# Performance work log

Hardware: AMD Instinct MI355X
Metric: run time of the kernel (lower is better)

## Reference

```python
import jax, jax.numpy as jnp
import numpy as np

BASE = 257
HASH_MOD = 4096
WINDOWS = (2, 4, 8, 16)
MATCH_OFFSETS = (1, 2, 4, 8)
CHUNK = 32
EPS_LN = 1e-5


def _shift_right(x, k):
    # (B,T) -> shifted right by k along time, zero-filled
    B, T = x.shape
    return jnp.concatenate([jnp.zeros((B, k), x.dtype), x[:, :T - k]], axis=1)


def _rolling_hashes(chars):
    # polynomial rolling hash over each window size, mod HASH_MOD -> (B,T,S) int32
    c = chars.astype(jnp.int32)
    hs = []
    for w in WINDOWS:
        acc = jnp.zeros_like(c)
        p = 1
        for j in range(w):  # small fixed loop (<=16)
            acc = acc + _shift_right(c, j) * p
            p = (p * BASE) % HASH_MOD
        hs.append(acc % HASH_MOD)
    return jnp.stack(hs, axis=2)


def _match_features(chars):
    feats = []
    for k in MATCH_OFFSETS:
        m = (chars == _shift_right(chars, k)).astype(jnp.float32)
        m = m.at[:, :k].set(0.0)
        feats.append(m)
    return jnp.stack(feats, axis=-1)  # (B,T,n_match)


def _layer_norm(x, g, b):
    mu = jnp.mean(x, axis=-1, keepdims=True)
    var = jnp.mean((x - mu) ** 2, axis=-1, keepdims=True)
    return (x - mu) * jax.lax.rsqrt(var + EPS_LN) * g + b


def _forward(chars, emb_byte, hash_tables, Wq, bq, conv_w, conv_b, Win, b_in,
             Wg, bg, Wi, bi, Wo, bo, ln_g, ln_b, mlp_w, mlp_b, Wout, bout):
    B, T = chars.shape
    byte_emb = emb_byte[chars]                       # (B,T,Eb)
    hidx = _rolling_hashes(chars)                    # (B,T,S)
    scale_embeds = jnp.stack(
        [hash_tables[s][hidx[:, :, s]] for s in range(len(WINDOWS))], axis=2
    )                                                # (B,T,S,E)
    # scale attention: query from byte embedding, softmax over scales
    E = scale_embeds.shape[-1]
    q = byte_emb @ Wq + bq                           # (B,T,E)
    scores = jnp.einsum('bte,btse->bts', q, scale_embeds) / jnp.sqrt(jnp.float32(E))
    w = jax.nn.softmax(scores, axis=-1)
    hash_feat = jnp.einsum('bts,btse->bte', w, scale_embeds)
    # causal depthwise conv + silu
    C = hash_feat.shape[-1]
    kk = conv_w.shape[-1]
    ht = jnp.moveaxis(hash_feat, 1, 2)               # (B,C,T)
    ht = jnp.pad(ht, ((0, 0), (0, 0), (kk - 1, 0)))
    ht = jax.lax.conv_general_dilated(
        ht, conv_w, window_strides=(1,), padding='VALID',
        dimension_numbers=('NCH', 'OIH', 'NCH'), feature_group_count=C)
    hash_feat = jax.nn.silu(jnp.moveaxis(ht + conv_b[None, :, None], 2, 1))
    mf = _match_features(chars)
    feat = jnp.concatenate([byte_emb, hash_feat, mf], axis=-1)
    h = jax.nn.silu(feat @ Win + b_in)               # (B,T,H)
    # TinyScan: chunked log-space gated scan, carry across chunks via lax.scan
    gates = jax.nn.sigmoid(h @ Wg + bg)              # (B,T,S)
    drive = (1.0 - gates) * (h @ Wi + bi)
    S = gates.shape[-1]
    nC = T // CHUNK
    g = gates.reshape(B, nC, CHUNK, S).transpose(1, 0, 2, 3)
    d = drive.reshape(B, nC, CHUNK, S).transpose(1, 0, 2, 3)

    def step(hc, ab):
        a, b = ab                                    # (B,K,S)
        log_a = jnp.log(jnp.maximum(a, 1e-6))
        cum_a = jnp.exp(jnp.cumsum(log_a, axis=1))
        inv = 1.0 / jnp.maximum(cum_a, 1e-8)
        cum_wb = jnp.cumsum(b * inv, axis=1)
        out = cum_a * (hc[:, None, :] + cum_wb)
        return out[:, -1], out

    _, states = jax.lax.scan(step, jnp.zeros((B, S), h.dtype), (g, d))
    states = states.transpose(1, 0, 2, 3).reshape(B, T, S)
    h = _layer_norm(h + states @ Wo + bo, ln_g, ln_b)
    # residual MLP blocks: x + silu(Linear(x))
    for l in range(mlp_w.shape[0]):
        h = h + jax.nn.silu(h @ mlp_w[l] + mlp_b[l])
    return h @ Wout + bout                           # (B,T,V)


def setup_inputs() -> dict:
    key = jax.random.key(0)
    ks = jax.random.split(key, 12)
    B, T, V = 8, 8192, 256
    EB, E, H, SS, KC, NM, NR = 64, 64, 512, 32, 4, 4, 3
    feat = EB + E + NM

    def lin(k, i, o):
        return (jax.random.normal(k, (i, o), jnp.float32) / np.sqrt(i)).astype(jnp.float32)

    return {
        'chars': jax.random.randint(ks[0], (B, T), 0, V),
        'emb_byte': jax.random.normal(ks[1], (V, EB), jnp.float32) * 0.02,
        'hash_tables': jax.random.normal(ks[2], (len(WINDOWS), HASH_MOD, E), jnp.float32) * 0.02,
        'Wq': lin(ks[3], EB, E), 'bq': jnp.zeros((E,), jnp.float32),
        'conv_w': jax.random.normal(ks[4], (E, 1, KC), jnp.float32) * 0.2,
        'conv_b': jnp.zeros((E,), jnp.float32),
        'Win': lin(ks[5], feat, H), 'b_in': jnp.zeros((H,), jnp.float32),
        'Wg': lin(ks[6], H, SS), 'bg': jnp.zeros((SS,), jnp.float32),
        'Wi': lin(ks[7], H, SS), 'bi': jnp.zeros((SS,), jnp.float32),
        'Wo': lin(ks[8], SS, H), 'bo': jnp.zeros((H,), jnp.float32),
        'ln_g': jnp.ones((H,), jnp.float32), 'ln_b': jnp.zeros((H,), jnp.float32),
        'mlp_w': jax.random.normal(ks[9], (NR, H, H), jnp.float32) / np.sqrt(H),
        'mlp_b': jnp.zeros((NR, H), jnp.float32),
        'Wout': lin(ks[10], H, V), 'bout': jnp.zeros((V,), jnp.float32),
    }


def reference(chars, emb_byte, hash_tables, Wq, bq, conv_w, conv_b, Win, b_in,
              Wg, bg, Wi, bi, Wo, bo, ln_g, ln_b, mlp_w, mlp_b, Wout, bout):
    return _forward(chars, emb_byte, hash_tables, Wq, bq, conv_w, conv_b, Win, b_in,
                    Wg, bg, Wi, bi, Wo, bo, ln_g, ln_b, mlp_w, mlp_b, Wout, bout)
```

## Files before the change

### kernel.cpp

```cpp
#include <hip/hip_runtime.h>
#include <hip/hip_bf16.h>
#include <math.h>

#define B_ 8
#define T_ 8192
#define V_ 256
#define EB_ 64
#define E_ 64
#define H_ 512
#define SS_ 32
#define FEATP_ 192
#define NCH_ 256
#define CHUNK_ 32

typedef __attribute__((ext_vector_type(8))) short bf8;
typedef __attribute__((ext_vector_type(16))) float accv;

#define AS1(p) (__attribute__((address_space(1))) void*)(void*)(p)
#define AS3(p) (__attribute__((address_space(3))) void*)(void*)(p)

__device__ __forceinline__ float silu_f(float x) { return x / (1.0f + expf(-x)); }
__device__ __forceinline__ float sigm_f(float x) { return 1.0f / (1.0f + expf(-x)); }
__device__ __forceinline__ float bf2f(__hip_bfloat16 v) { return __bfloat162float(v); }
__device__ __forceinline__ __hip_bfloat16 f2bf(float v) { return __float2bfloat16(v); }
__device__ __forceinline__ float us2f(ushort u) {
    union { float f; unsigned int u32; } c; c.u32 = ((unsigned int)u) << 16; return c.f;
}
__device__ __forceinline__ ushort f2us(float v) {
    __hip_bfloat16 t = __float2bfloat16(v);
    return *reinterpret_cast<ushort*>(&t);
}

#define CD_ROW(r, lane) (((r) & 3) + 8 * ((r) >> 2) + 4 * ((lane) >> 5))

__device__ __forceinline__ int xcd_swz(int bid, int nwg) {
    return (bid & 7) * (nwg >> 3) + (bid >> 3);
}

template <int KD>
__device__ __forceinline__ void mm256(const ushort* __restrict__ Ab,
                                      const ushort* __restrict__ Bb,
                                      int m0, int n0, accv (&acc)[4][2]) {
    constexpr int NT = KD / 64;
    __shared__ __align__(1024) ushort lA[32768];
    __shared__ __align__(1024) ushort lB[32768];
    const int tid  = threadIdx.x;
    const int lane = tid & 63;
    const int w    = tid >> 6;
    const int wm   = w >> 2, wn = w & 3;

    const int srow = tid & 255;
    const int sh   = tid >> 8;
    const ushort* gA = Ab + (size_t)(m0 + srow) * KD + sh * 8;
    const ushort* gB = Bb + (size_t)(n0 + srow) * KD + sh * 8;
    const int doff  = w * 512;
    const int raoff = (lane >> 5) * 2048 + (128 * wm + (lane & 31)) * 8;
    const int rboff = (lane >> 5) * 2048 + (64 * wn + (lane & 31)) * 8;

#define STG(slot, f, koff)                                                                          \
    do {                                                                                            \
        __builtin_amdgcn_global_load_lds(AS1(gA + (koff) + (f) * 16),                               \
                                         AS3(&lA[(slot) * 16384 + (f) * 4096 + doff]), 16, 0, 0);   \
        __builtin_amdgcn_global_load_lds(AS1(gB + (koff) + (f) * 16),                               \
                                         AS3(&lB[(slot) * 16384 + (f) * 4096 + doff]), 16, 0, 0);   \
    } while (0)

#define WAITBAR(n)                                                    \
    do {                                                              \
        asm volatile("s_waitcnt vmcnt(" #n ")" ::: "memory");         \
        __builtin_amdgcn_s_barrier();                                 \
        __builtin_amdgcn_sched_barrier(0);                            \
    } while (0)

#define PH(slot, f)                                                                                \
    do {                                                                                           \
        const ushort* pa = &lA[(slot) * 16384 + (f) * 4096 + raoff];                               \
        const ushort* pb = &lB[(slot) * 16384 + (f) * 4096 + rboff];                               \
        bf8 b0v = *(const bf8*)(pb);                                                               \
        bf8 b1v = *(const bf8*)(pb + 256);                                                         \
        bf8 a0v = *(const bf8*)(pa);                                                               \
        bf8 a1v = *(const bf8*)(pa + 256);                                                         \
        bf8 a2v = *(const bf8*)(pa + 512);                                                         \
        bf8 a3v = *(const bf8*)(pa + 768);                                                         \
        __builtin_amdgcn_s_setprio(1);                                                             \
        acc[0][0] = __builtin_amdgcn_mfma_f32_32x32x16_bf16(a0v, b0v, acc[0][0], 0, 0, 0);         \
        acc[0][1] = __builtin_amdgcn_mfma_f32_32x32x16_bf16(a0v, b1v, acc[0][1], 0, 0, 0);         \
        acc[1][0] = __builtin_amdgcn_mfma_f32_32x32x16_bf16(a1v, b0v, acc[1][0], 0, 0, 0);         \
        acc[1][1] = __builtin_amdgcn_mfma_f32_32x32x16_bf16(a1v, b1v, acc[1][1], 0, 0, 0);         \
        acc[2][0] = __builtin_amdgcn_mfma_f32_32x32x16_bf16(a2v, b0v, acc[2][0], 0, 0, 0);         \
        acc[2][1] = __builtin_amdgcn_mfma_f32_32x32x16_bf16(a2v, b1v, acc[2][1], 0, 0, 0);         \
        acc[3][0] = __builtin_amdgcn_mfma_f32_32x32x16_bf16(a3v, b0v, acc[3][0], 0, 0, 0);         \
        acc[3][1] = __builtin_amdgcn_mfma_f32_32x32x16_bf16(a3v, b1v, acc[3][1], 0, 0, 0);         \
        __builtin_amdgcn_s_setprio(0);                                                             \
    } while (0)

    STG(0, 0, 0); STG(0, 1, 0); STG(0, 2, 0); STG(0, 3, 0);
    int kt = 64;
    for (int t = 0; t < NT - 1; ++t) {
        const int slot = t & 1;
        STG(slot ^ 1, 0, kt); WAITBAR(8); PH(slot, 0);
        STG(slot ^ 1, 1, kt); WAITBAR(8); PH(slot, 1);
        STG(slot ^ 1, 2, kt); WAITBAR(8); PH(slot, 2);
        STG(slot ^ 1, 3, kt); WAITBAR(8); PH(slot, 3);
        kt += 64;
    }
    {
        const int ls = (NT - 1) & 1;
        WAITBAR(6); PH(ls, 0);
        WAITBAR(4); PH(ls, 1);
        WAITBAR(2); PH(ls, 2);
        WAITBAR(0); PH(ls, 3);
    }
#undef STG
#undef WAITBAR
#undef PH
}

__device__ __forceinline__ void zero_acc8(accv (&acc)[4][2]) {
#pragma unroll
    for (int i = 0; i < 4; i++)
#pragma unroll
        for (int j = 0; j < 2; j++)
#pragma unroll
            for (int r = 0; r < 16; r++) acc[i][j][r] = 0.0f;
}

__global__ __launch_bounds__(512, 2) void k_mlp256(const __hip_bfloat16* __restrict__ hin,
                                                   const __hip_bfloat16* __restrict__ Wt,
                                                   const float* __restrict__ bias,
                                                   __hip_bfloat16* __restrict__ hout) {
    accv acc[4][2];
    zero_acc8(acc);
    int wg = xcd_swz(blockIdx.x, 512);
    int m0 = (wg >> 1) * 256, n0 = (wg & 1) * 256;
    int lane = threadIdx.x & 63, w = threadIdx.x >> 6, wm = w >> 2, wn = w & 3;
    mm256<H_>((const ushort*)hin, (const ushort*)Wt, m0, n0, acc);
#pragma unroll
    for (int fr = 0; fr < 4; fr++)
#pragma unroll
        for (int fc = 0; fc < 2; fc++) {
            int col = n0 + 64 * wn + 32 * fc + (lane & 31);
            float bv = bias[col];
#pragma unroll
            for (int r = 0; r < 16; r++) {
                int row = m0 + 128 * wm + 32 * fr + CD_ROW(r, lane);
                float v = acc[fr][fc][r] + bv;
                float res = bf2f(hin[(size_t)row * H_ + col]);
                hout[(size_t)row * H_ + col] = f2bf(res + silu_f(v));
            }
        }
}

__global__ __launch_bounds__(512, 2) void k_win256(const __hip_bfloat16* __restrict__ featb,
                                                   const __hip_bfloat16* __restrict__ Wt,
                                                   const float* __restrict__ bias,
                                                   __hip_bfloat16* __restrict__ hb) {
    accv acc[4][2];
    zero_acc8(acc);
    int wg = xcd_swz(blockIdx.x, 512);
    int m0 = (wg >> 1) * 256, n0 = (wg & 1) * 256;
    int lane = threadIdx.x & 63, w = threadIdx.x >> 6, wm = w >> 2, wn = w & 3;
    mm256<FEATP_>((const ushort*)featb, (const ushort*)Wt, m0, n0, acc);
#pragma unroll
    for (int fr = 0; fr < 4; fr++)
#pragma unroll
        for (int fc = 0; fc < 2; fc++) {
            int col = n0 + 64 * wn + 32 * fc + (lane & 31);
            float bv = bias[col];
#pragma unroll
            for (int r = 0; r < 16; r++) {
                int row = m0 + 128 * wm + 32 * fr + CD_ROW(r, lane);
                hb[(size_t)row * H_ + col] = f2bf(silu_f(acc[fr][fc][r] + bv));
            }
        }
}

__global__ __launch_bounds__(512, 2) void k_out256(const __hip_bfloat16* __restrict__ hb,
                                                   const __hip_bfloat16* __restrict__ Wt,
                                                   const float* __restrict__ bout,
                                                   float* __restrict__ out) {
    accv acc[4][2];
    zero_acc8(acc);
    int wg = xcd_swz(blockIdx.x, 256);
    int m0 = wg * 256;
    int lane = threadIdx.x & 63, w = threadIdx.x >> 6, wm = w >> 2, wn = w & 3;
    mm256<H_>((const ushort*)hb, (const ushort*)Wt, m0, 0, acc);
#pragma unroll
    for (int fr = 0; fr < 4; fr++)
#pragma unroll
        for (int fc = 0; fc < 2; fc++) {
            int col = 64 * wn + 32 * fc + (lane & 31);
            float bv = bout[col];
#pragma unroll
            for (int r = 0; r < 16; r++) {
                int row = m0 + 128 * wm + 32 * fr + CD_ROW(r, lane);
                out[(size_t)row * V_ + col] = acc[fr][fc][r] + bv;
            }
        }
}

template <int KD>
__device__ __forceinline__ void mm128(const __hip_bfloat16* __restrict__ A,
                                      const __hip_bfloat16* __restrict__ Wt,
                                      int m0, int n0, accv (&acc)[2][2]) {
    __shared__ __align__(16) ushort lA[128 * 32];
    __shared__ __align__(16) ushort lB[128 * 32];
    int tid = threadIdx.x;
    int lane = tid & 63, w = tid >> 6;
    int wm = w & 1, wn = w >> 1;
    int c0 = w * 128 + lane;
    int c1 = c0 + 64;
    const ushort* Ab = (const ushort*)A;
    const ushort* Bb = (const ushort*)Wt;
    const ushort* gA0 = Ab + (size_t)(m0 + (c0 >> 2)) * KD + (c0 & 3) * 8;
    const ushort* gA1 = Ab + (size_t)(m0 + (c1 >> 2)) * KD + (c1 & 3) * 8;
    const ushort* gB0 = Bb + (size_t)(n0 + (c0 >> 2)) * KD + (c0 & 3) * 8;
    const ushort* gB1 = Bb + (size_t)(n0 + (c1 >> 2)) * KD + (c1 & 3) * 8;
    ushort* dA0 = &lA[(w * 128) * 8];
    ushort* dA1 = &lA[(w * 128 + 64) * 8];
    ushort* dB0 = &lB[(w * 128) * 8];
    ushort* dB1 = &lB[(w * 128 + 64) * 8];
    const ushort* pa = &lA[(64 * wm + (lane & 31)) * 32 + (lane >> 5) * 8];
    const ushort* pb = &lB[(64 * wn + (lane & 31)) * 32 + (lane >> 5) * 8];

    for (int kt = 0; kt < KD; kt += 32) {
        __builtin_amdgcn_global_load_lds(AS1(gA0 + kt), AS3(dA0), 16, 0, 0);
        __builtin_amdgcn_global_load_lds(AS1(gA1 + kt), AS3(dA1), 16, 0, 0);
        __builtin_amdgcn_global_load_lds(AS1(gB0 + kt), AS3(dB0), 16, 0, 0);
        __builtin_amdgcn_global_load_lds(AS1(gB1 + kt), AS3(dB1), 16, 0, 0);
        __syncthreads();
#pragma unroll
        for (int ks = 0; ks < 2; ks++) {
            bf8 a0 = *(const bf8*)(pa + ks * 16);
            bf8 a1 = *(const bf8*)(pa + 32 * 32 + ks * 16);
            bf8 b0 = *(const bf8*)(pb + ks * 16);
            bf8 b1 = *(const bf8*)(pb + 32 * 32 + ks * 16);
            acc[0][0] = __builtin_amdgcn_mfma_f32_32x32x16_bf16(a0, b0, acc[0][0], 0, 0, 0);
            acc[0][1] = __builtin_amdgcn_mfma_f32_32x32x16_bf16(a0, b1, acc[0][1], 0, 0, 0);
            acc[1][0] = __builtin_amdgcn_mfma_f32_32x32x16_bf16(a1, b0, acc[1][0], 0, 0, 0);
            acc[1][1] = __builtin_amdgcn_mfma_f32_32x32x16_bf16(a1, b1, acc[1][1], 0, 0, 0);
        }
        __syncthreads();
    }
}

__device__ __forceinline__ void zero_acc(accv (&acc)[2][2]) {
#pragma unroll
    for (int i = 0; i < 2; i++)
#pragma unroll
        for (int j = 0; j < 2; j++)
#pragma unroll
            for (int r = 0; r < 16; r++) acc[i][j][r] = 0.0f;
}

__global__ __launch_bounds__(256) void k_womm(const __hip_bfloat16* __restrict__ states_bf,
                                              const __hip_bfloat16* __restrict__ Wt_wo,
                                              const float* __restrict__ bo,
                                              const __hip_bfloat16* __restrict__ hb,
                                              __hip_bfloat16* __restrict__ tmp) {
    accv acc[2][2];
    zero_acc(acc);
    int lane = threadIdx.x & 63, w = threadIdx.x >> 6, wm = w & 1, wn = w >> 1;
    int m0 = blockIdx.x * 128, n0 = blockIdx.y * 128;
    mm128<SS_>(states_bf, Wt_wo, m0, n0, acc);
#pragma unroll
    for (int i = 0; i < 2; i++)
#pragma unroll
        for (int j = 0; j < 2; j++) {
            int col = n0 + 64 * wn + 32 * j + (lane & 31);
            float bv = bo[col];
#pragma unroll
            for (int r = 0; r < 16; r++) {
                int row = m0 + 64 * wm + 32 * i + CD_ROW(r, lane);
                float res = bf2f(hb[(size_t)row * H_ + col]);
                tmp[(size_t)row * H_ + col] = f2bf(res + acc[i][j][r] + bv);
            }
        }
}

__global__ __launch_bounds__(256) void k_ln(const __hip_bfloat16* __restrict__ tmp,
                                            const float* __restrict__ ln_g,
                                            const float* __restrict__ ln_b,
                                            __hip_bfloat16* __restrict__ hb) {
    int wave = threadIdx.x >> 6, lane = threadIdx.x & 63;
    int token = blockIdx.x * 4 + wave;
    const ushort* row = (const ushort*)(tmp + (size_t)token * H_) + lane * 8;
    bf8 xv = *(const bf8*)row;
    float x[8];
    float sm = 0.f, sq = 0.f;
#pragma unroll
    for (int i = 0; i < 8; i++) {
        x[i] = us2f((ushort)xv[i]);
        sm += x[i];
        sq += x[i] * x[i];
    }
#pragma unroll
    for (int off = 32; off; off >>= 1) {
        sm += __shfl_xor(sm, off, 64);
        sq += __shfl_xor(sq, off, 64);
    }
    float mu = sm * (1.0f / 512.0f);
    float var = sq * (1.0f / 512.0f) - mu * mu;
    float rstd = rsqrtf(fmaxf(var, 0.0f) + 1e-5f);
    float4 g0 = *(const float4*)(ln_g + lane * 8);
    float4 g1 = *(const float4*)(ln_g + lane * 8 + 4);
    float4 b0 = *(const float4*)(ln_b + lane * 8);
    float4 b1 = *(const float4*)(ln_b + lane * 8 + 4);
    float gg[8] = {g0.x, g0.y, g0.z, g0.w, g1.x, g1.y, g1.z, g1.w};
    float bb[8] = {b0.x, b0.y, b0.z, b0.w, b1.x, b1.y, b1.z, b1.w};
    bf8 o;
#pragma unroll
    for (int i = 0; i < 8; i++) o[i] = (short)f2us((x[i] - mu) * rstd * gg[i] + bb[i]);
    *(bf8*)((ushort*)(hb + (size_t)token * H_) + lane * 8) = o;
}

__global__ __launch_bounds__(256) void k_gates_mfma(const __hip_bfloat16* __restrict__ hb,
                                                    const __hip_bfloat16* __restrict__ Wt_gd,
                                                    const float* __restrict__ bg,
                                                    const float* __restrict__ bi,
                                                    float* __restrict__ gates,
                                                    float* __restrict__ drive) {
    __shared__ __align__(16) ushort lA[256 * 32];
    __shared__ __align__(16) ushort lB[64 * 32];
    int tid = threadIdx.x, lane = tid & 63, w = tid >> 6;
    int m0 = blockIdx.x * 256;
    accv acc[2][2];
    zero_acc(acc);
    const ushort* Ab = (const ushort*)hb;
    const ushort* Bb = (const ushort*)Wt_gd;
    const ushort* pa = &lA[(64 * w + (lane & 31)) * 32 + (lane >> 5) * 8];
    const ushort* pb = &lB[((lane & 31)) * 32 + (lane >> 5) * 8];
    int cb = w * 64 + lane;
    const ushort* gB = Bb + (size_t)(cb >> 2) * H_ + (cb & 3) * 8;
    for (int kt = 0; kt < H_; kt += 32) {
#pragma unroll
        for (int j = 0; j < 4; j++) {
            int c = w * 256 + j * 64 + lane;
            __builtin_amdgcn_global_load_lds(
                AS1(Ab + (size_t)(m0 + (c >> 2)) * H_ + (c & 3) * 8 + kt),
                AS3(&lA[(w * 256 + j * 64) * 8]), 16, 0, 0);
        }
        __builtin_amdgcn_global_load_lds(AS1(gB + kt), AS3(&lB[(w * 64) * 8]), 16, 0, 0);
        __syncthreads();
#pragma unroll
        for (int ks = 0; ks < 2; ks++) {
            bf8 a0 = *(const bf8*)(pa + ks * 16);
            bf8 a1 = *(const bf8*)(pa + 32 * 32 + ks * 16);
            bf8 b0 = *(const bf8*)(pb + ks * 16);
            bf8 b1 = *(const bf8*)(pb + 32 * 32 + ks * 16);
            acc[0][0] = __builtin_amdgcn_mfma_f32_32x32x16_bf16(a0, b0, acc[0][0], 0, 0, 0);
            acc[0][1] = __builtin_amdgcn_mfma_f32_32x32x16_bf16(a0, b1, acc[0][1], 0, 0, 0);
            acc[1][0] = __builtin_amdgcn_mfma_f32_32x32x16_bf16(a1, b0, acc[1][0], 0, 0, 0);
            acc[1][1] = __builtin_amdgcn_mfma_f32_32x32x16_bf16(a1, b1, acc[1][1], 0, 0, 0);
        }
        __syncthreads();
    }
    int c = lane & 31;
    float bgv = bg[c], biv = bi[c];
#pragma unroll
    for (int i = 0; i < 2; i++)
#pragma unroll
        for (int r = 0; r < 16; r++) {
            int row = m0 + 64 * w + 32 * i + CD_ROW(r, lane);
            float g = sigm_f(acc[i][0][r] + bgv);
            float d = (1.0f - g) * (acc[i][1][r] + biv);
            gates[(size_t)row * SS_ + c] = g;
            drive[(size_t)row * SS_ + c] = d;
        }
}

__global__ __launch_bounds__(256) void k_prep_w(const float* __restrict__ mlp_w,
                                                const float* __restrict__ Wout,
                                                const float* __restrict__ Win,
                                                const float* __restrict__ Wg,
                                                const float* __restrict__ Wi,
                                                const float* __restrict__ Wo,
                                                const float* __restrict__ Wq,
                                                const float* __restrict__ bq,
                                                const float* __restrict__ emb_byte,
                                                __hip_bfloat16* __restrict__ Wt_mlp,
                                                __hip_bfloat16* __restrict__ Wt_out,
                                                __hip_bfloat16* __restrict__ Wt_win,
                                                __hip_bfloat16* __restrict__ Wt_gd,
                                                __hip_bfloat16* __restrict__ Wt_wo,
                                                float* __restrict__ Qtab) {
    int idx = blockIdx.x * 256 + threadIdx.x;
    if (idx < 786432) {
        int l = idx >> 18, rem = idx & 262143;
        int n = rem >> 9, k = rem & 511;
        Wt_mlp[idx] = f2bf(mlp_w[l * 262144 + k * 512 + n]);
    } else if (idx < 917504) {
        int rem = idx - 786432;
        int n = rem >> 9, k = rem & 511;
        Wt_out[rem] = f2bf(Wout[k * 256 + n]);
    } else if (idx < 1015808) {
        int rem = idx - 917504;
        int n = rem / FEATP_, k = rem % FEATP_;
        Wt_win[rem] = f2bf(k < 132 ? Win[k * 512 + n] : 0.0f);
    } else if (idx < 1048576) {
        int rem = idx - 1015808;
        int n = rem >> 9, k = rem & 511;
        Wt_gd[rem] = f2bf(n < 32 ? Wg[k * 32 + n] : Wi[k * 32 + (n - 32)]);
    } else if (idx < 1064960) {
        int rem = idx - 1048576;
        int n = rem >> 5, k = rem & 31;
        Wt_wo[rem] = f2bf(Wo[k * H_ + n]);
    } else if (idx < 1081344) {
        int rem = idx - 1064960;
        int c = rem >> 6, e = rem & 63;
        float a = bq[e];
#pragma unroll 8
        for (int k = 0; k < 64; k++) a += emb_byte[c * 64 + k] * Wq[k * 64 + e];
        Qtab[rem] = a * 0.125f;
    }
}

__global__ __launch_bounds__(256) void k_token_feats(
    const int* __restrict__ chars, const float* __restrict__ emb_byte,
    const float* __restrict__ hash_tables, const float* __restrict__ Qtab,
    __hip_bfloat16* __restrict__ featb, float* __restrict__ hfpre) {
    int wave = threadIdx.x >> 6, lane = threadIdx.x & 63;
    int token = blockIdx.x * 4 + wave;
    int t = token & (T_ - 1);
    int b = token >> 13;
    const int* crow = chars + b * T_;
    int cv[16];
#pragma unroll
    for (int j = 0; j < 16; j++) cv[j] = (t >= j) ? crow[t - j] : 0;
    int acc = 0;
    int hidx[4];
#pragma unroll
    for (int j = 0; j < 16; j++) {
        acc += cv[j] * (1 + 256 * j);
        if (j == 1) hidx[0] = acc & 4095;
        if (j == 3) hidx[1] = acc & 4095;
        if (j == 7) hidx[2] = acc & 4095;
        if (j == 15) hidx[3] = acc & 4095;
    }
    int c0 = cv[0];
    float be = emb_byte[c0 * EB_ + lane];
    float q = Qtab[c0 * 64 + lane];
    float se[4];
#pragma unroll
    for (int s = 0; s < 4; s++) se[s] = hash_tables[(s * 4096 + hidx[s]) * E_ + lane];
    float sc[4];
#pragma unroll
    for (int s = 0; s < 4; s++) {
        float v = q * se[s];
#pragma unroll
        for (int off = 32; off; off >>= 1) v += __shfl_xor(v, off, 64);
        sc[s] = v;
    }
    float mx = fmaxf(fmaxf(sc[0], sc[1]), fmaxf(sc[2], sc[3]));
    float w0 = expf(sc[0] - mx), w1 = expf(sc[1] - mx), w2 = expf(sc[2] - mx), w3 = expf(sc[3] - mx);
    float inv = 1.0f / (w0 + w1 + w2 + w3);
    float hf = (w0 * se[0] + w1 * se[1] + w2 * se[2] + w3 * se[3]) * inv;
    featb[(size_t)token * FEATP_ + lane] = f2bf(be);
    hfpre[(size_t)token * E_ + lane] = hf;
    if (lane < 32) {
        float m = 0.0f;
        if (lane < 4) {
            int k = 1 << lane;
            m = (t >= k && c0 == cv[k]) ? 1.0f : 0.0f;
        }
        featb[(size_t)token * FEATP_ + 128 + lane] = f2bf(m);
    } else {
        featb[(size_t)token * FEATP_ + 128 + lane] = f2bf(0.0f);
    }
}

__global__ __launch_bounds__(256) void k_conv(
    const float* __restrict__ hfpre, const float* __restrict__ conv_w,
    const float* __restrict__ conv_b, __hip_bfloat16* __restrict__ featb) {
    int idx = blockIdx.x * 256 + threadIdx.x;
    int e = idx & 63;
    int bt = idx >> 6;
    int t = bt & (T_ - 1);
    float acc = conv_b[e];
#pragma unroll
    for (int k = 0; k < 4; k++) {
        int tt = t - 3 + k;
        if (tt >= 0) acc += hfpre[(size_t)(bt - 3 + k) * E_ + e] * conv_w[e * 4 + k];
    }
    featb[(size_t)bt * FEATP_ + 64 + e] = f2bf(silu_f(acc));
}

__global__ __launch_bounds__(256) void k_chunk_ab(
    const float* __restrict__ gates, const float* __restrict__ drive,
    float* __restrict__ chA, float* __restrict__ chB) {
    int gid = blockIdx.x * 256 + threadIdx.x;
    int s = gid & 31;
    int n = (gid >> 5) & (NCH_ - 1);
    int b = gid >> 13;
    int base = (b * T_ + n * CHUNK_) * SS_ + s;
    float suml = 0.f, cum_wb = 0.f, cum_a = 1.f;
    for (int i = 0; i < CHUNK_; i++) {
        float g = gates[base + i * SS_];
        float d = drive[base + i * SS_];
        suml += logf(fmaxf(g, 1e-6f));
        cum_a = expf(suml);
        cum_wb += d / fmaxf(cum_a, 1e-8f);
    }
    chA[gid] = cum_a;
    chB[gid] = cum_a * cum_wb;
}

__global__ void k_chunk_scan(const float* __restrict__ chA, const float* __restrict__ chB,
                             float* __restrict__ chH) {
    int tid = threadIdx.x;
    int b = tid >> 5, s = tid & 31;
    const float* pA = chA + (size_t)b * NCH_ * SS_ + s;
    const float* pB = chB + (size_t)b * NCH_ * SS_ + s;
    float* pH = chH + (size_t)b * NCH_ * SS_ + s;
    float hc = 0.f;
    for (int n = 0; n < NCH_; n += 8) {
        float a[8], bb[8];
#pragma unroll
        for (int i = 0; i < 8; i++) {
            a[i] = pA[(n + i) * SS_];
            bb[i] = pB[(n + i) * SS_];
        }
#pragma unroll
        for (int i = 0; i < 8; i++) {
            pH[(n + i) * SS_] = hc;
            hc = a[i] * hc + bb[i];
        }
    }
}

__global__ __launch_bounds__(256) void k_states(
    const float* __restrict__ gates, const float* __restrict__ drive,
    const float* __restrict__ chH, __hip_bfloat16* __restrict__ states_bf) {
    int gid = blockIdx.x * 256 + threadIdx.x;
    int s = gid & 31;
    int n = (gid >> 5) & (NCH_ - 1);
    int b = gid >> 13;
    int base = (b * T_ + n * CHUNK_) * SS_ + s;
    float hc = chH[gid];
    float suml = 0.f, cum_wb = 0.f;
    for (int i = 0; i < CHUNK_; i++) {
        float g = gates[base + i * SS_];
        float d = drive[base + i * SS_];
        suml += logf(fmaxf(g, 1e-6f));
        float cum_a = expf(suml);
        cum_wb += d / fmaxf(cum_a, 1e-8f);
        states_bf[base + i * SS_] = f2bf(cum_a * (hc + cum_wb));
    }
}

extern "C" void kernel_launch(void* const* d_in, const int* in_sizes, int n_in,
                              void* d_out, int out_size, void* d_ws, size_t ws_size,
                              hipStream_t stream) {
    (void)in_sizes; (void)n_in; (void)out_size; (void)ws_size;
    const int*   chars       = (const int*)  d_in[0];
    const float* emb_byte    = (const float*)d_in[1];
    const float* hash_tables = (const float*)d_in[2];
    const float* Wq          = (const float*)d_in[3];
    const float* bq          = (const float*)d_in[4];
    const float* conv_w      = (const float*)d_in[5];
    const float* conv_b      = (const float*)d_in[6];
    const float* Win         = (const float*)d_in[7];
    const float* b_in        = (const float*)d_in[8];
    const float* Wg          = (const float*)d_in[9];
    const float* bg          = (const float*)d_in[10];
    const float* Wi          = (const float*)d_in[11];
    const float* bi          = (const float*)d_in[12];
    const float* Wo          = (const float*)d_in[13];
    const float* bo          = (const float*)d_in[14];
    const float* ln_g        = (const float*)d_in[15];
    const float* ln_b        = (const float*)d_in[16];
    const float* mlp_w       = (const float*)d_in[17];
    const float* mlp_b       = (const float*)d_in[18];
    const float* Wout        = (const float*)d_in[19];
    const float* bout        = (const float*)d_in[20];
    float* out = (float*)d_out;

    const size_t NTOK = (size_t)B_ * T_;
    char* p = (char*)d_ws;
    auto alloc = [&](size_t bytes) { void* r = (void*)p; p += (bytes + 255) & ~(size_t)255; return r; };
    __hip_bfloat16* featb = (__hip_bfloat16*)alloc(NTOK * FEATP_ * 2);
    float*          hfpre = (float*)alloc(NTOK * E_ * 4);
    __hip_bfloat16* hbA   = (__hip_bfloat16*)alloc(NTOK * H_ * 2);
    __hip_bfloat16* hbB   = (__hip_bfloat16*)alloc(NTOK * H_ * 2);
    float*          gates = (float*)alloc(NTOK * SS_ * 4);
    float*          drive = (float*)alloc(NTOK * SS_ * 4);
    __hip_bfloat16* states_bf = (__hip_bfloat16*)alloc(NTOK * SS_ * 2);
    float*          chA   = (float*)alloc((size_t)B_ * NCH_ * SS_ * 4);
    float*          chB   = (float*)alloc((size_t)B_ * NCH_ * SS_ * 4);
    float*          chH   = (float*)alloc((size_t)B_ * NCH_ * SS_ * 4);
    __hip_bfloat16* Wt_mlp= (__hip_bfloat16*)alloc(3 * 512 * 512 * 2);
    __hip_bfloat16* Wt_out= (__hip_bfloat16*)alloc(256 * 512 * 2);
    __hip_bfloat16* Wt_win= (__hip_bfloat16*)alloc(512 * FEATP_ * 2);
    __hip_bfloat16* Wt_gd = (__hip_bfloat16*)alloc(64 * 512 * 2);
    __hip_bfloat16* Wt_wo = (__hip_bfloat16*)alloc(512 * SS_ * 2);
    float*          Qtab  = (float*)alloc(256 * 64 * 4);

    k_prep_w<<<4224, 256, 0, stream>>>(mlp_w, Wout, Win, Wg, Wi, Wo, Wq, bq, emb_byte,
                                       Wt_mlp, Wt_out, Wt_win, Wt_gd, Wt_wo, Qtab);
    k_token_feats<<<NTOK / 4, 256, 0, stream>>>(chars, emb_byte, hash_tables, Qtab, featb, hfpre);
    k_conv<<<NTOK * E_ / 256, 256, 0, stream>>>(hfpre, conv_w, conv_b, featb);
    k_win256<<<512, 512, 0, stream>>>(featb, Wt_win, b_in, hbA);
    k_gates_mfma<<<NTOK / 256, 256, 0, stream>>>(hbA, Wt_gd, bg, bi, gates, drive);
    k_chunk_ab<<<B_ * NCH_ * SS_ / 256, 256, 0, stream>>>(gates, drive, chA, chB);
    k_chunk_scan<<<1, 256, 0, stream>>>(chA, chB, chH);
    k_states<<<B_ * NCH_ * SS_ / 256, 256, 0, stream>>>(gates, drive, chH, states_bf);
    k_womm<<<dim3(NTOK / 128, 4), 256, 0, stream>>>(states_bf, Wt_wo, bo, hbA, hbB);
    k_ln<<<NTOK / 4, 256, 0, stream>>>(hbB, ln_g, ln_b, hbA);
    k_mlp256<<<512, 512, 0, stream>>>(hbA, Wt_mlp, mlp_b, hbB);
    k_mlp256<<<512, 512, 0, stream>>>(hbB, Wt_mlp + 262144, mlp_b + 512, hbA);
    k_mlp256<<<512, 512, 0, stream>>>(hbA, Wt_mlp + 524288, mlp_b + 1024, hbB);
    k_out256<<<256, 512, 0, stream>>>(hbB, Wt_out, bout, out);
}
```

Before: 645.4 us.

## Use XOR-swizzled row-major LDS tiles and per-k-tile barriers in mm256 GEMM

Restructures the GEMM's LDS staging so each wave loads 32 full rows of a 64-wide K tile with an XOR swizzle on the column group, and reads MFMA operands through matching swizzled offsets. This replaces the earlier four sub-phase staging with a single stage per 64-K tile followed by four MFMA phases between two barriers. The aim is to cut LDS bank conflicts and the number of waits and barriers per tile. In exchange it gives up the finer-grained overlap between loading and MFMA work, and adds a second barrier per iteration.

Measured after the change: 521.2 us. -19.2%, faster.

```diff
diff --git a/kernel.cpp b/kernel.cpp
--- a/kernel.cpp
+++ b/kernel.cpp
@@ -49,40 +49,50 @@
     const int w    = tid >> 6;
     const int wm   = w >> 2, wn = w & 3;
 
-    const int srow = tid & 255;
-    const int sh   = tid >> 8;
-    const ushort* gA = Ab + (size_t)(m0 + srow) * KD + sh * 8;
-    const ushort* gB = Bb + (size_t)(n0 + srow) * KD + sh * 8;
-    const int doff  = w * 512;
-    const int raoff = (lane >> 5) * 2048 + (128 * wm + (lane & 31)) * 8;
-    const int rboff = (lane >> 5) * 2048 + (64 * wn + (lane & 31)) * 8;
-
-#define STG(slot, f, koff)                                                                          \
-    do {                                                                                            \
-        __builtin_amdgcn_global_load_lds(AS1(gA + (koff) + (f) * 16),                               \
-                                         AS3(&lA[(slot) * 16384 + (f) * 4096 + doff]), 16, 0, 0);   \
-        __builtin_amdgcn_global_load_lds(AS1(gB + (koff) + (f) * 16),                               \
-                                         AS3(&lB[(slot) * 16384 + (f) * 4096 + doff]), 16, 0, 0);   \
+    const int lrow = lane >> 3;
+    const int lcg  = (lane & 7) ^ lrow;
+    const ushort* gA = Ab + (size_t)(m0 + w * 32 + lrow) * KD + lcg * 8;
+    const ushort* gB = Bb + (size_t)(n0 + w * 32 + lrow) * KD + lcg * 8;
+    const int dstw = w * 2048;
+
+    const int swz  = (lane & 7) << 4;
+    const int kh16 = (lane >> 5) * 16;
+    int oK[4];
+#pragma unroll
+    for (int ks = 0; ks < 4; ks++) oK[ks] = ((ks * 32 + kh16) ^ swz) >> 1;
+    const int rowA = (128 * wm + (lane & 31)) * 64;
+    const int rowB = (64 * wn + (lane & 31)) * 64;
+
+#define STG8(slot, kt)                                                                             \
+    do {                                                                                           \
+        __builtin_amdgcn_global_load_lds(AS1(gA + (kt)),                                           \
+                                         AS3(&lA[(slot) * 16384 + dstw + 0 * 512]), 16, 0, 0);     \
+        __builtin_amdgcn_global_load_lds(AS1(gB + (kt)),                                           \
+                                         AS3(&lB[(slot) * 16384 + dstw + 0 * 512]), 16, 0, 0);     \
+        __builtin_amdgcn_global_load_lds(AS1(gA + (size_t)8 * KD + (kt)),                          \
+                                         AS3(&lA[(slot) * 16384 + dstw + 1 * 512]), 16, 0, 0);     \
+        __builtin_amdgcn_global_load_lds(AS1(gB + (size_t)8 * KD + (kt)),                          \
+                                         AS3(&lB[(slot) * 16384 + dstw + 1 * 512]), 16, 0, 0);     \
+        __builtin_amdgcn_global_load_lds(AS1(gA + (size_t)16 * KD + (kt)),                         \
+                                         AS3(&lA[(slot) * 16384 + dstw + 2 * 512]), 16, 0, 0);     \
+        __builtin_amdgcn_global_load_lds(AS1(gB + (size_t)16 * KD + (kt)),                         \
+                                         AS3(&lB[(slot) * 16384 + dstw + 2 * 512]), 16, 0, 0);     \
+        __builtin_amdgcn_global_load_lds(AS1(gA + (size_t)24 * KD + (kt)),                         \
+                                         AS3(&lA[(slot) * 16384 + dstw + 3 * 512]), 16, 0, 0);     \
+        __builtin_amdgcn_global_load_lds(AS1(gB + (size_t)24 * KD + (kt)),                         \
+                                         AS3(&lB[(slot) * 16384 + dstw + 3 * 512]), 16, 0, 0);     \
     } while (0)
 
-#define WAITBAR(n)                                                    \
-    do {                                                              \
-        asm volatile("s_waitcnt vmcnt(" #n ")" ::: "memory");         \
-        __builtin_amdgcn_s_barrier();                                 \
-        __builtin_amdgcn_sched_barrier(0);                            \
-    } while (0)
-
-#define PH(slot, f)                                                                                \
+#define PH(slot, ks)                                                                               \
     do {                                                                                           \
-        const ushort* pa = &lA[(slot) * 16384 + (f) * 4096 + raoff];                               \
-        const ushort* pb = &lB[(slot) * 16384 + (f) * 4096 + rboff];                               \
+        const ushort* pa = &lA[(slot) * 16384 + rowA + oK[ks]];                                    \
+        const ushort* pb = &lB[(slot) * 16384 + rowB + oK[ks]];                                    \
         bf8 b0v = *(const bf8*)(pb);                                                               \
-        bf8 b1v = *(const bf8*)(pb + 256);                                                         \
+        bf8 b1v = *(const bf8*)(pb + 2048);                                                        \
         bf8 a0v = *(const bf8*)(pa);                                                               \
-        bf8 a1v = *(const bf8*)(pa + 256);                                                         \
-        bf8 a2v = *(const bf8*)(pa + 512);                                                         \
-        bf8 a3v = *(const bf8*)(pa + 768);                                                         \
-        __builtin_amdgcn_s_setprio(1);                                                             \
+        bf8 a1v = *(const bf8*)(pa + 2048);                                                        \
+        bf8 a2v = *(const bf8*)(pa + 4096);                                                        \
+        bf8 a3v = *(const bf8*)(pa + 6144);                                                        \
         acc[0][0] = __builtin_amdgcn_mfma_f32_32x32x16_bf16(a0v, b0v, acc[0][0], 0, 0, 0);         \
         acc[0][1] = __builtin_amdgcn_mfma_f32_32x32x16_bf16(a0v, b1v, acc[0][1], 0, 0, 0);         \
         acc[1][0] = __builtin_amdgcn_mfma_f32_32x32x16_bf16(a1v, b0v, acc[1][0], 0, 0, 0);         \
@@ -91,28 +101,31 @@
         acc[2][1] = __builtin_amdgcn_mfma_f32_32x32x16_bf16(a2v, b1v, acc[2][1], 0, 0, 0);         \
         acc[3][0] = __builtin_amdgcn_mfma_f32_32x32x16_bf16(a3v, b0v, acc[3][0], 0, 0, 0);         \
         acc[3][1] = __builtin_amdgcn_mfma_f32_32x32x16_bf16(a3v, b1v, acc[3][1], 0, 0, 0);         \
-        __builtin_amdgcn_s_setprio(0);                                                             \
     } while (0)
 
-    STG(0, 0, 0); STG(0, 1, 0); STG(0, 2, 0); STG(0, 3, 0);
-    int kt = 64;
+    STG8(0, 0);
+#pragma unroll
     for (int t = 0; t < NT - 1; ++t) {
         const int slot = t & 1;
-        STG(slot ^ 1, 0, kt); WAITBAR(8); PH(slot, 0);
-        STG(slot ^ 1, 1, kt); WAITBAR(8); PH(slot, 1);
-        STG(slot ^ 1, 2, kt); WAITBAR(8); PH(slot, 2);
-        STG(slot ^ 1, 3, kt); WAITBAR(8); PH(slot, 3);
-        kt += 64;
-    }
+        STG8(slot ^ 1, (t + 1) * 64);
+        asm volatile("s_waitcnt vmcnt(8)" ::: "memory");
+        __builtin_amdgcn_s_barrier();
+        __builtin_amdgcn_sched_barrier(0);
+        __builtin_amdgcn_s_setprio(1);
+        PH(slot, 0); PH(slot, 1); PH(slot, 2); PH(slot, 3);
+        __builtin_amdgcn_s_setprio(0);
+        __builtin_amdgcn_s_barrier();
+    }
+    asm volatile("s_waitcnt vmcnt(0)" ::: "memory");
+    __builtin_amdgcn_s_barrier();
+    __builtin_amdgcn_sched_barrier(0);
     {
         const int ls = (NT - 1) & 1;
-        WAITBAR(6); PH(ls, 0);
-        WAITBAR(4); PH(ls, 1);
-        WAITBAR(2); PH(ls, 2);
-        WAITBAR(0); PH(ls, 3);
-    }
-#undef STG
-#undef WAITBAR
+        __builtin_amdgcn_s_setprio(1);
+        PH(ls, 0); PH(ls, 1); PH(ls, 2); PH(ls, 3);
+        __builtin_amdgcn_s_setprio(0);
+    }
+#undef STG8
 #undef PH
 }
 
```
